# Kernel optimization log

Hardware: AMD Instinct MI355X
Metric: run time of the kernel (lower is better)

Reference implementation:

```python
import jax, jax.numpy as jnp
import numpy as np
import math

B, S, D, H = 2048, 32, 1024, 16
DK = D // H
EPS = 1e-5

def setup_inputs() -> dict:
    key = jax.random.key(0)
    ks = jax.random.split(key, 8)
    w_scale = 0.02  # realistic init scale for linear weights
    # Weights stored as (d_in, d_out): y = x @ W + b (same math as torch x @ W.T)
    return {
        "x":  jax.random.normal(ks[0], (B, S, D), jnp.float32),
        "ln_g": jnp.ones((D,), jnp.float32),
        "ln_b": jnp.zeros((D,), jnp.float32),
        "wq": jax.random.normal(ks[1], (D, D), jnp.float32) * w_scale,
        "bq": jnp.zeros((D,), jnp.float32),
        "wk": jax.random.normal(ks[2], (D, D), jnp.float32) * w_scale,
        "bk": jnp.zeros((D,), jnp.float32),
        "wv": jax.random.normal(ks[3], (D, D), jnp.float32) * w_scale,
        "bv": jnp.zeros((D,), jnp.float32),
        "wo": jax.random.normal(ks[4], (D, D), jnp.float32) * w_scale,
        "bo": jnp.zeros((D,), jnp.float32),
        "rel_bias": jax.random.normal(ks[5], (H, 32, 32), jnp.float32),
    }

def reference(x, ln_g, ln_b, wq, bq, wk, bk, wv, bv, wo, bo, rel_bias):
    b, s, d = x.shape
    h = rel_bias.shape[0]
    dk = d // h
    residual = x
    # LayerNorm (eps=1e-5)
    mu = jnp.mean(x, axis=-1, keepdims=True)
    var = jnp.mean(jnp.square(x - mu), axis=-1, keepdims=True)
    xn = (x - mu) * jax.lax.rsqrt(var + EPS) * ln_g + ln_b
    # QKV projections -> [b, h, s, dk]
    def split_heads(t):
        return t.reshape(b, s, h, dk).transpose(0, 2, 1, 3)
    Q = split_heads(xn @ wq + bq)
    K = split_heads(xn @ wk + bk)
    V = split_heads(xn @ wv + bv)
    scores = jnp.einsum('bhqd,bhkd->bhqk', Q, K) / jnp.sqrt(jnp.float32(dk))
    if s <= 32:  # static at trace time, matching the torch branch
        scores = scores + rel_bias[:, :s, :s][None]
    attn = jax.nn.softmax(scores, axis=-1)
    ctx = jnp.einsum('bhqk,bhkd->bhqd', attn, V)
    ctx = ctx.transpose(0, 2, 1, 3).reshape(b, s, d)
    out = ctx @ wo + bo  # dropout is identity in eval
    return residual + out
```

## Files before the change

kernel.cpp:

```cpp
#include <hip/hip_runtime.h>
#include <stdint.h>


typedef __attribute__((ext_vector_type(8))) short bf16x8;
typedef __attribute__((ext_vector_type(4))) float f32x4;
typedef __attribute__((ext_vector_type(16))) float f32x16;

__device__ __forceinline__ float bf2f(unsigned short u) {
    return __uint_as_float(((unsigned)u) << 16);
}
__device__ __forceinline__ unsigned short f2bf(float f) {
    unsigned u = __float_as_uint(f);
    u += 0x7FFFu + ((u >> 16) & 1u);
    return (unsigned short)(u >> 16);
}
__device__ __forceinline__ uint4 pack8(const float* f) {
    uint4 u;
    u.x = (unsigned)f2bf(f[0]) | ((unsigned)f2bf(f[1]) << 16);
    u.y = (unsigned)f2bf(f[2]) | ((unsigned)f2bf(f[3]) << 16);
    u.z = (unsigned)f2bf(f[4]) | ((unsigned)f2bf(f[5]) << 16);
    u.w = (unsigned)f2bf(f[6]) | ((unsigned)f2bf(f[7]) << 16);
    return u;
}

typedef __attribute__((address_space(3))) unsigned lds_u32;
typedef const __attribute__((address_space(1))) unsigned glb_u32;
__device__ __forceinline__ void gld16(const void* g, void* l) {
    __builtin_amdgcn_global_load_lds((glb_u32*)g, (lds_u32*)l, 16, 0, 0);
}

__global__ __launch_bounds__(256) void lnw_kernel(
    const float* __restrict__ x, const float* __restrict__ gg,
    const float* __restrict__ bb, unsigned short* __restrict__ xn,
    const float* __restrict__ wq, const float* __restrict__ wk,
    const float* __restrict__ wv, const float* __restrict__ wo,
    unsigned short* __restrict__ wcatT, unsigned short* __restrict__ woT)
{
    __shared__ unsigned short T[64 * 72];
    if (blockIdx.x >= 16384) {
        int bid = blockIdx.x - 16384;
        int p = bid >> 8;
        int t = bid & 255;
        int k0 = (t >> 4) * 64, n0 = (t & 15) * 64;
        const float* src = (p == 0) ? wq : (p == 1) ? wk : (p == 2) ? wv : wo;
        unsigned short* dst = (p < 3) ? (wcatT + (size_t)p * 1048576) : woT;
        int tid = threadIdx.x;
#pragma unroll
        for (int it = 0; it < 2; it++) {
            int flat = it * 2048 + tid * 8;
            int r = flat >> 6, c = flat & 63;
            const float* s4 = src + (size_t)(k0 + r) * 1024 + n0 + c;
            float4 u0 = *(const float4*)s4;
            float4 u1 = *(const float4*)(s4 + 4);
            float f[8] = {u0.x, u0.y, u0.z, u0.w, u1.x, u1.y, u1.z, u1.w};
            *(uint4*)&T[r * 72 + c] = pack8(f);
        }
        __syncthreads();
#pragma unroll
        for (int it = 0; it < 2; it++) {
            int flat = it * 2048 + tid * 8;
            int rn = flat >> 6, ck = flat & 63;
            unsigned short v[8];
#pragma unroll
            for (int j = 0; j < 8; j++) v[j] = T[(ck + j) * 72 + rn];
            uint4 u;
            u.x = (unsigned)v[0] | ((unsigned)v[1] << 16);
            u.y = (unsigned)v[2] | ((unsigned)v[3] << 16);
            u.z = (unsigned)v[4] | ((unsigned)v[5] << 16);
            u.w = (unsigned)v[6] | ((unsigned)v[7] << 16);
            *(uint4*)(dst + (size_t)(n0 + rn) * 1024 + k0 + ck) = u;
        }
        return;
    }
    int l = threadIdx.x & 63;
    size_t row = (size_t)blockIdx.x * 4 + (threadIdx.x >> 6);
    const float* xr = x + row * 1024;
    float f0[8], f1[8];
    *(float4*)&f0[0] = *(const float4*)(xr + l * 8);
    *(float4*)&f0[4] = *(const float4*)(xr + l * 8 + 4);
    *(float4*)&f1[0] = *(const float4*)(xr + 512 + l * 8);
    *(float4*)&f1[4] = *(const float4*)(xr + 512 + l * 8 + 4);
    float s = 0.f, s2 = 0.f;
#pragma unroll
    for (int j = 0; j < 8; j++) { s += f0[j] + f1[j]; s2 += f0[j] * f0[j] + f1[j] * f1[j]; }
#pragma unroll
    for (int m = 1; m < 64; m <<= 1) { s += __shfl_xor(s, m); s2 += __shfl_xor(s2, m); }
    float mu = s * (1.f / 1024.f);
    float var = s2 * (1.f / 1024.f) - mu * mu;
    float rs = rsqrtf(var + 1e-5f);
    float fg0[8], fg1[8], fb0[8], fb1[8];
    *(float4*)&fg0[0] = *(const float4*)(gg + l * 8);
    *(float4*)&fg0[4] = *(const float4*)(gg + l * 8 + 4);
    *(float4*)&fg1[0] = *(const float4*)(gg + 512 + l * 8);
    *(float4*)&fg1[4] = *(const float4*)(gg + 512 + l * 8 + 4);
    *(float4*)&fb0[0] = *(const float4*)(bb + l * 8);
    *(float4*)&fb0[4] = *(const float4*)(bb + l * 8 + 4);
    *(float4*)&fb1[0] = *(const float4*)(bb + 512 + l * 8);
    *(float4*)&fb1[4] = *(const float4*)(bb + 512 + l * 8 + 4);
    float o0[8], o1[8];
#pragma unroll
    for (int j = 0; j < 8; j++) {
        o0[j] = (f0[j] - mu) * rs * fg0[j] + fb0[j];
        o1[j] = (f1[j] - mu) * rs * fg1[j] + fb1[j];
    }
    *(uint4*)(xn + row * 1024 + l * 8) = pack8(o0);
    *(uint4*)(xn + row * 1024 + 512 + l * 8) = pack8(o1);
}

#define FENCE asm volatile("" ::: "memory")
#define BARRIER do { FENCE; __builtin_amdgcn_s_barrier(); FENCE; } while (0)
#define WAIT_LGKM0 do { asm volatile("s_waitcnt lgkmcnt(0)" ::: "memory"); \
                        __builtin_amdgcn_sched_barrier(0); } while (0)
#define VMCNT(n) asm volatile("s_waitcnt vmcnt(" #n ")" ::: "memory")

#define FQ_SA(buf) (LDSU + (buf) * 8192)
#define FQ_SB(buf) (LDSU + 16384 + (buf) * 12288)
#define QS_OFF 0
#define KS_OFF 9216
#define VT_OFF 18432
#define PS_OFF 28672

#define ASTG(buf, g, koff) gld16(Ag + (size_t)(g) * 32768 + (koff), \
                                 FQ_SA(buf) + ((g) * 32 + w * 8) * 64)
#define BSTG(buf, p, c, koff) gld16(((p) == 0 ? Bgq : (p) == 1 ? Bgk : Bgv) + (size_t)(c) * 32768 + (koff), \
                                    FQ_SB(buf) + ((p) * 64 + (c) * 32 + w * 8) * 64)

#define FLDA(buf, q, ks) (*(const bf16x8*)&FQ_SA(buf)[ \
    (wm * 64 + (q) * 16 + (l & 15)) * 64 + ((((ks) * 32) + khi) ^ aswz)])
#define FLDB(buf, cf, ks) (*(const bf16x8*)&FQ_SB(buf)[ \
    (wn * 96 + (cf) * 16 + (l & 15)) * 64 + ((((ks) * 32) + khi) ^ aswz)])

#define MFMA_HEX(q) do { \
    _Pragma("unroll") \
    for (int cf = 0; cf < 6; cf++) { \
        acc[q][cf] = __builtin_amdgcn_mfma_f32_16x16x32_bf16(aF0, bF[cf][0], acc[q][cf], 0, 0, 0); \
        acc[q][cf] = __builtin_amdgcn_mfma_f32_16x16x32_bf16(aF1, bF[cf][1], acc[q][cf], 0, 0, 0); \
    } } while (0)

#define FPHASE(buf, q, STAGE_STMT, TAIL_STMT) do { \
    bf16x8 aF0 = FLDA(buf, q, 0), aF1 = FLDA(buf, q, 1); \
    if ((q) == 0) { \
        _Pragma("unroll") \
        for (int cf = 0; cf < 6; cf++) { bF[cf][0] = FLDB(buf, cf, 0); bF[cf][1] = FLDB(buf, cf, 1); } \
    } \
    STAGE_STMT; \
    BARRIER; \
    WAIT_LGKM0; \
    __builtin_amdgcn_s_setprio(1); \
    MFMA_HEX(q); \
    __builtin_amdgcn_s_setprio(0); \
    TAIL_STMT; \
    BARRIER; \
} while (0)

__global__ __launch_bounds__(256, 2) void fqa2_kernel(
    const unsigned short* __restrict__ A, const unsigned short* __restrict__ wcatT,
    const float* __restrict__ bq, const float* __restrict__ bk,
    const float* __restrict__ bv, const float* __restrict__ rb,
    unsigned short* __restrict__ ctx)
{
    __shared__ __align__(16) unsigned short LDSU[40960];
    int bx = blockIdx.x;
    int h  = ((bx & 7) << 1) | ((bx >> 3) & 1);
    int mp = bx >> 4;
    int m0 = mp * 128;
    int tid = threadIdx.x, l = tid & 63, w = tid >> 6;
    int wm = w >> 1, wn = w & 1;
    int khi = (l >> 4) * 8;
    int aswz = (l & 7) * 8;
    int swzc = ((l & 7) ^ (l >> 3)) * 8;

    const unsigned short* Ag  = A + (size_t)(m0 + w * 8 + (l >> 3)) * 1024 + swzc;
    const unsigned short* Bgq = wcatT + (size_t)(h * 64 + w * 8 + (l >> 3)) * 1024 + swzc;
    const unsigned short* Bgk = Bgq + 1048576ull;
    const unsigned short* Bgv = Bgq + 2097152ull;

    f32x4 acc[4][6];
#pragma unroll
    for (int i = 0; i < 4; i++)
#pragma unroll
        for (int j = 0; j < 6; j++)
#pragma unroll
            for (int v = 0; v < 4; v++) acc[i][j][v] = 0.f;

    bf16x8 bF[6][2];

    ASTG(0, 0, 0); ASTG(0, 1, 0); ASTG(0, 2, 0); ASTG(0, 3, 0);
    BSTG(0, 0, 0, 0); BSTG(0, 0, 1, 0); BSTG(0, 1, 0, 0);
    BSTG(0, 1, 1, 0); BSTG(0, 2, 0, 0); BSTG(0, 2, 1, 0);
    BSTG(1, 0, 0, 64); BSTG(1, 0, 1, 64); BSTG(1, 1, 0, 64);
    BSTG(1, 1, 1, 64); BSTG(1, 2, 0, 64); BSTG(1, 2, 1, 64);
    VMCNT(6);
    BARRIER;

    for (int it = 0; it < 7; ++it) {
        int ko1 = (2 * it + 1) * 64, ko2 = (2 * it + 2) * 64, ko3 = (2 * it + 3) * 64;
        FPHASE(0, 0, do { ASTG(1, 0, ko1); ASTG(1, 1, ko1); } while (0), (void)0);
        FPHASE(0, 1, do { ASTG(1, 2, ko1); ASTG(1, 3, ko1); } while (0), (void)0);
        FPHASE(0, 2, do { BSTG(0, 0, 0, ko2); BSTG(0, 0, 1, ko2); BSTG(0, 1, 0, ko2); } while (0), (void)0);
        FPHASE(0, 3, do { BSTG(0, 1, 1, ko2); BSTG(0, 2, 0, ko2); BSTG(0, 2, 1, ko2); } while (0), VMCNT(6));
        FPHASE(1, 0, do { ASTG(0, 0, ko2); ASTG(0, 1, ko2); } while (0), (void)0);
        FPHASE(1, 1, do { ASTG(0, 2, ko2); ASTG(0, 3, ko2); } while (0), (void)0);
        FPHASE(1, 2, do { BSTG(1, 0, 0, ko3); BSTG(1, 0, 1, ko3); BSTG(1, 1, 0, ko3); } while (0), (void)0);
        FPHASE(1, 3, do { BSTG(1, 1, 1, ko3); BSTG(1, 2, 0, ko3); BSTG(1, 2, 1, ko3); } while (0), VMCNT(6));
    }
    FPHASE(0, 0, do { ASTG(1, 0, 960); ASTG(1, 1, 960); } while (0), (void)0);
    FPHASE(0, 1, do { ASTG(1, 2, 960); ASTG(1, 3, 960); } while (0), (void)0);
    FPHASE(0, 2, (void)0, (void)0);
    FPHASE(0, 3, (void)0, VMCNT(0));
    FPHASE(1, 0, (void)0, (void)0);
    FPHASE(1, 1, (void)0, (void)0);
    FPHASE(1, 2, (void)0, (void)0);
    FPHASE(1, 3, (void)0, (void)0);
    __builtin_amdgcn_sched_barrier(0);

#pragma unroll
    for (int cf = 0; cf < 6; cf++) {
        int colg = wn * 96 + cf * 16 + (l & 15);
        int seg = colg >> 6;
        int cseg = colg & 63;
        const float* bp = (seg == 0) ? bq : (seg == 1) ? bk : bv;
        float bias = bp[h * 64 + cseg];
#pragma unroll
        for (int ai = 0; ai < 4; ai++) {
#pragma unroll
            for (int v = 0; v < 4; v++) {
                int row = wm * 64 + ai * 16 + (l >> 4) * 4 + v;
                unsigned short val = f2bf(acc[ai][cf][v] + bias);
                if (seg == 0)      LDSU[QS_OFF + row * 72 + cseg] = val;
                else if (seg == 1) LDSU[KS_OFF + row * 72 + cseg] = val;
                else               LDSU[VT_OFF + (((row >> 5) << 6) + cseg) * 40 + (row & 31)] = val;
            }
        }
    }
    __syncthreads();

    {
        int col = l & 31, hi = l >> 5;
        f32x16 s;
#pragma unroll
        for (int i = 0; i < 16; i++) s[i] = 0.f;
#pragma unroll
        for (int t = 0; t < 4; t++) {
            bf16x8 aQ = *(const bf16x8*)&LDSU[QS_OFF + (w * 32 + col) * 72 + t * 16 + hi * 8];
            bf16x8 bK = *(const bf16x8*)&LDSU[KS_OFF + (w * 32 + col) * 72 + t * 16 + hi * 8];
            s = __builtin_amdgcn_mfma_f32_32x32x16_bf16(aQ, bK, s, 0, 0, 0);
        }
        const float* rbh = rb + h * 1024;
        unsigned short* ps = LDSU + PS_OFF + w * 1280;
#pragma unroll
        for (int r = 0; r < 16; r++) {
            int m = (r & 3) + 8 * (r >> 2) + 4 * hi;
            float v = s[r] * 0.125f + rbh[m * 32 + col];
            float mx = v;
#pragma unroll
            for (int msk = 1; msk < 32; msk <<= 1) mx = fmaxf(mx, __shfl_xor(mx, msk));
            float e = __expf(v - mx);
            float sm = e;
#pragma unroll
            for (int msk = 1; msk < 32; msk <<= 1) sm += __shfl_xor(sm, msk);
            ps[m * 40 + col] = f2bf(e / sm);
        }
        bf16x8 pa0 = *(const bf16x8*)&ps[col * 40 + hi * 8];
        bf16x8 pa1 = *(const bf16x8*)&ps[col * 40 + 16 + hi * 8];
        size_t rowb = ((size_t)mp * 4 + w) * 32;
#pragma unroll
        for (int c2 = 0; c2 < 2; c2++) {
            bf16x8 vb0 = *(const bf16x8*)&LDSU[VT_OFF + (w * 64 + c2 * 32 + col) * 40 + hi * 8];
            bf16x8 vb1 = *(const bf16x8*)&LDSU[VT_OFF + (w * 64 + c2 * 32 + col) * 40 + 16 + hi * 8];
            f32x16 o;
#pragma unroll
            for (int i = 0; i < 16; i++) o[i] = 0.f;
            o = __builtin_amdgcn_mfma_f32_32x32x16_bf16(pa0, vb0, o, 0, 0, 0);
            o = __builtin_amdgcn_mfma_f32_32x32x16_bf16(pa1, vb1, o, 0, 0, 0);
#pragma unroll
            for (int r = 0; r < 16; r++) {
                int m = (r & 3) + 8 * (r >> 2) + 4 * hi;
                ctx[(rowb + m) * 1024 + h * 64 + c2 * 32 + col] = f2bf(o[r]);
            }
        }
    }
}

#define SAp(buf) (LDSB + (buf) * 16384)
#define SBp(buf) (LDSB + 32768 + (buf) * 16384)

#define STG(gb, hh, kcol, ldsreg) do { \
    const unsigned short* _g = (gb) + (size_t)((hh) * 128) * 1024 + (kcol); \
    unsigned short* _d = (ldsreg) + ((hh) * 128 + w * 8) * 64; \
    gld16(_g, _d); gld16(_g + 64 * 1024, _d + 64 * 64); } while (0)

#define LDA(buf, q, rfq, ks) (*(const bf16x8*)&SAp(buf)[ \
    (wm * 128 + (q) * 32 + (rfq) * 16 + (l & 15)) * 64 + ((((ks) * 32) + khi) ^ aswz)])
#define LDB(buf, cf, ks) (*(const bf16x8*)&SBp(buf)[ \
    (wn * 64 + (cf) * 16 + (l & 15)) * 64 + ((((ks) * 32) + khi) ^ aswz)])

#define MFMA_QUAD(q) do { \
    _Pragma("unroll") \
    for (int cf = 0; cf < 4; cf++) { \
        acc[(q)*2+0][cf] = __builtin_amdgcn_mfma_f32_16x16x32_bf16(aF00, bF[cf][0], acc[(q)*2+0][cf], 0, 0, 0); \
        acc[(q)*2+0][cf] = __builtin_amdgcn_mfma_f32_16x16x32_bf16(aF01, bF[cf][1], acc[(q)*2+0][cf], 0, 0, 0); \
        acc[(q)*2+1][cf] = __builtin_amdgcn_mfma_f32_16x16x32_bf16(aF10, bF[cf][0], acc[(q)*2+1][cf], 0, 0, 0); \
        acc[(q)*2+1][cf] = __builtin_amdgcn_mfma_f32_16x16x32_bf16(aF11, bF[cf][1], acc[(q)*2+1][cf], 0, 0, 0); \
    } } while (0)

#define PHASE(buf, q, STAGE_STMT, TAIL_STMT) do { \
    bf16x8 aF00 = LDA(buf, q, 0, 0), aF01 = LDA(buf, q, 0, 1); \
    bf16x8 aF10 = LDA(buf, q, 1, 0), aF11 = LDA(buf, q, 1, 1); \
    if ((q) == 0) { \
        _Pragma("unroll") \
        for (int cf = 0; cf < 4; cf++) { bF[cf][0] = LDB(buf, cf, 0); bF[cf][1] = LDB(buf, cf, 1); } \
    } \
    STAGE_STMT; \
    BARRIER; \
    WAIT_LGKM0; \
    __builtin_amdgcn_s_setprio(1); \
    MFMA_QUAD(q); \
    __builtin_amdgcn_s_setprio(0); \
    TAIL_STMT; \
    BARRIER; \
} while (0)

__global__ __launch_bounds__(512, 2) void gemm8res(
    const unsigned short* __restrict__ A, const unsigned short* __restrict__ Bt,
    const float* __restrict__ bz0, const float* __restrict__ resid,
    float* __restrict__ out, int NTL)
{
    __shared__ __align__(16) unsigned short LDSB[65536];
    int cpx = gridDim.x >> 3;
    int bid = (blockIdx.x & 7) * cpx + (blockIdx.x >> 3);
    int mt = bid / NTL, ntl = bid % NTL;
    int m0 = mt * 256, n0 = ntl * 256;
    int tid = threadIdx.x, l = tid & 63, w = tid >> 6;
    int wm = w >> 2, wn = w & 3;
    int khi = (l >> 4) * 8;
    int aswz = (l & 7) * 8;

    const unsigned short* Ag = A + (size_t)(m0 + w * 8 + (l >> 3)) * 1024 + ((l & 7) ^ (l >> 3)) * 8;
    const unsigned short* Bg = Bt + (size_t)(n0 + w * 8 + (l >> 3)) * 1024 + ((l & 7) ^ (l >> 3)) * 8;
    unsigned short* sA0 = SAp(0);
    unsigned short* sA1 = SAp(1);
    unsigned short* sB0 = SBp(0);
    unsigned short* sB1 = SBp(1);

    f32x4 acc[8][4];
#pragma unroll
    for (int i = 0; i < 8; i++)
#pragma unroll
        for (int j = 0; j < 4; j++)
#pragma unroll
            for (int v = 0; v < 4; v++) acc[i][j][v] = 0.f;

    bf16x8 bF[4][2];

    STG(Ag, 0, 0, sA0); STG(Ag, 1, 0, sA0);
    STG(Bg, 0, 0, sB0); STG(Bg, 1, 0, sB0);
    STG(Bg, 0, 64, sB1); STG(Bg, 1, 64, sB1);
    VMCNT(4);
    BARRIER;

    for (int it = 0; it < 7; ++it) {
        int koff = it * 128;
        PHASE(0, 0, STG(Ag, 0, koff + 64, sA1), (void)0);
        PHASE(0, 1, STG(Ag, 1, koff + 64, sA1), (void)0);
        PHASE(0, 2, STG(Bg, 0, koff + 128, sB0), (void)0);
        PHASE(0, 3, STG(Bg, 1, koff + 128, sB0), VMCNT(4));
        PHASE(1, 0, STG(Ag, 0, koff + 128, sA0), (void)0);
        PHASE(1, 1, STG(Ag, 1, koff + 128, sA0), (void)0);
        PHASE(1, 2, STG(Bg, 0, koff + 192, sB1), (void)0);
        PHASE(1, 3, STG(Bg, 1, koff + 192, sB1), VMCNT(4));
    }
    PHASE(0, 0, STG(Ag, 0, 960, sA1), (void)0);
    PHASE(0, 1, STG(Ag, 1, 960, sA1), (void)0);
    PHASE(0, 2, (void)0, (void)0);
    PHASE(0, 3, (void)0, VMCNT(0));
    PHASE(1, 0, (void)0, (void)0);
    PHASE(1, 1, (void)0, (void)0);
    PHASE(1, 2, (void)0, (void)0);
    PHASE(1, 3, (void)0, (void)0);
    __builtin_amdgcn_sched_barrier(0);

    float* Cf = (float*)LDSB;
    int gcol = n0 + l * 4;
    float4 bzv = *(const float4*)(bz0 + gcol);
#pragma unroll
    for (int pass = 0; pass < 2; pass++) {
        __syncthreads();
#pragma unroll
        for (int rfq = 0; rfq < 4; rfq++) {
            int rf = pass * 4 + rfq;
#pragma unroll
            for (int cf = 0; cf < 4; cf++) {
                int c0 = wn * 64 + cf * 16 + (l & 15);
                int c4 = c0 >> 2, ce = c0 & 3;
#pragma unroll
                for (int v = 0; v < 4; v++) {
                    int rl = wm * 64 + rfq * 16 + (l >> 4) * 4 + v;
                    Cf[rl * 256 + ((c4 ^ (rl & 7)) << 2) + ce] = acc[rf][cf][v];
                }
            }
        }
        __syncthreads();
#pragma unroll
        for (int rb4 = 0; rb4 < 4; rb4++) {
            float4 rz[4], cv[4];
#pragma unroll
            for (int k = 0; k < 4; k++) {
                int rr = (rb4 * 4 + k) * 8 + w;
                int grow = m0 + (rr & 63) + ((rr >> 6) << 7) + pass * 64;
                rz[k] = *(const float4*)(resid + (size_t)grow * 1024 + gcol);
            }
#pragma unroll
            for (int k = 0; k < 4; k++) {
                int rr = (rb4 * 4 + k) * 8 + w;
                cv[k] = *(const float4*)&Cf[rr * 256 + ((l ^ (rr & 7)) << 2)];
            }
#pragma unroll
            for (int k = 0; k < 4; k++) {
                int rr = (rb4 * 4 + k) * 8 + w;
                int grow = m0 + (rr & 63) + ((rr >> 6) << 7) + pass * 64;
                float4 o;
                o.x = cv[k].x + bzv.x + rz[k].x;
                o.y = cv[k].y + bzv.y + rz[k].y;
                o.z = cv[k].z + bzv.z + rz[k].z;
                o.w = cv[k].w + bzv.w + rz[k].w;
                *(float4*)(out + (size_t)grow * 1024 + gcol) = o;
            }
        }
    }
}

extern "C" void kernel_launch(void* const* d_in, const int* in_sizes, int n_in,
                              void* d_out, int out_size, void* d_ws, size_t ws_size,
                              hipStream_t stream)
{
    const float* x  = (const float*)d_in[0];
    const float* lg = (const float*)d_in[1];
    const float* lb = (const float*)d_in[2];
    const float* wq = (const float*)d_in[3];
    const float* bq = (const float*)d_in[4];
    const float* wk = (const float*)d_in[5];
    const float* bk = (const float*)d_in[6];
    const float* wv = (const float*)d_in[7];
    const float* bv = (const float*)d_in[8];
    const float* wo = (const float*)d_in[9];
    const float* bo = (const float*)d_in[10];
    const float* rb = (const float*)d_in[11];
    float* out = (float*)d_out;
    unsigned short* ws = (unsigned short*)d_ws;

    unsigned short* wcatT = ws;
    unsigned short* woT   = wcatT + 3145728;
    unsigned short* xn    = woT + 1048576;
    unsigned short* ctx   = xn + 67108864ull;

    lnw_kernel<<<dim3(17408), dim3(256), 0, stream>>>(
        x, lg, lb, xn, wq, wk, wv, wo, wcatT, woT);

    fqa2_kernel<<<dim3(8192), dim3(256), 0, stream>>>(xn, wcatT, bq, bk, bv, rb, ctx);

    gemm8res<<<dim3(1024), dim3(512), 0, stream>>>(ctx, woT, bo, x, out, 4);
}
```

Measured before the change: 761.8 us.

## Merge GEMM phases into paired quads and stage ctx output through LDS

The fused QKV+attention kernel now handles two A row-quads per phase. This halves the number of barrier-separated phases in the K loop and issues larger groups of global-to-LDS staging loads per phase. The attention epilogue computes both 32-column PV halves together, writes them to the warp's V^T LDS region, and then stores ctx with 16-byte coalesced writes instead of scattered 2-byte stores. Two A fragments stay live at once, which raises register pressure, and reusing the V^T region for output assumes each warp only touches its own slice.

Result: faster. 744.5 us (-2.3%).

```diff
diff --git a/kernel.cpp b/kernel.cpp
--- a/kernel.cpp
+++ b/kernel.cpp
@@ -130,16 +130,17 @@
 #define FLDB(buf, cf, ks) (*(const bf16x8*)&FQ_SB(buf)[ \
     (wn * 96 + (cf) * 16 + (l & 15)) * 64 + ((((ks) * 32) + khi) ^ aswz)])
 
-#define MFMA_HEX(q) do { \
+#define MFMA_HEX2(q, a0, a1) do { \
     _Pragma("unroll") \
     for (int cf = 0; cf < 6; cf++) { \
-        acc[q][cf] = __builtin_amdgcn_mfma_f32_16x16x32_bf16(aF0, bF[cf][0], acc[q][cf], 0, 0, 0); \
-        acc[q][cf] = __builtin_amdgcn_mfma_f32_16x16x32_bf16(aF1, bF[cf][1], acc[q][cf], 0, 0, 0); \
+        acc[q][cf] = __builtin_amdgcn_mfma_f32_16x16x32_bf16(a0, bF[cf][0], acc[q][cf], 0, 0, 0); \
+        acc[q][cf] = __builtin_amdgcn_mfma_f32_16x16x32_bf16(a1, bF[cf][1], acc[q][cf], 0, 0, 0); \
     } } while (0)
 
-#define FPHASE(buf, q, STAGE_STMT, TAIL_STMT) do { \
-    bf16x8 aF0 = FLDA(buf, q, 0), aF1 = FLDA(buf, q, 1); \
-    if ((q) == 0) { \
+#define FPHASE2(buf, q0, LOADB, STAGE_STMT, TAIL_STMT) do { \
+    bf16x8 aF0 = FLDA(buf, q0, 0), aF1 = FLDA(buf, q0, 1); \
+    bf16x8 aG0 = FLDA(buf, (q0) + 1, 0), aG1 = FLDA(buf, (q0) + 1, 1); \
+    if (LOADB) { \
         _Pragma("unroll") \
         for (int cf = 0; cf < 6; cf++) { bF[cf][0] = FLDB(buf, cf, 0); bF[cf][1] = FLDB(buf, cf, 1); } \
     } \
@@ -147,7 +148,8 @@
     BARRIER; \
     WAIT_LGKM0; \
     __builtin_amdgcn_s_setprio(1); \
-    MFMA_HEX(q); \
+    MFMA_HEX2(q0, aF0, aF1); \
+    MFMA_HEX2((q0) + 1, aG0, aG1); \
     __builtin_amdgcn_s_setprio(0); \
     TAIL_STMT; \
     BARRIER; \
@@ -195,23 +197,27 @@
 
     for (int it = 0; it < 7; ++it) {
         int ko1 = (2 * it + 1) * 64, ko2 = (2 * it + 2) * 64, ko3 = (2 * it + 3) * 64;
-        FPHASE(0, 0, do { ASTG(1, 0, ko1); ASTG(1, 1, ko1); } while (0), (void)0);
-        FPHASE(0, 1, do { ASTG(1, 2, ko1); ASTG(1, 3, ko1); } while (0), (void)0);
-        FPHASE(0, 2, do { BSTG(0, 0, 0, ko2); BSTG(0, 0, 1, ko2); BSTG(0, 1, 0, ko2); } while (0), (void)0);
-        FPHASE(0, 3, do { BSTG(0, 1, 1, ko2); BSTG(0, 2, 0, ko2); BSTG(0, 2, 1, ko2); } while (0), VMCNT(6));
-        FPHASE(1, 0, do { ASTG(0, 0, ko2); ASTG(0, 1, ko2); } while (0), (void)0);
-        FPHASE(1, 1, do { ASTG(0, 2, ko2); ASTG(0, 3, ko2); } while (0), (void)0);
-        FPHASE(1, 2, do { BSTG(1, 0, 0, ko3); BSTG(1, 0, 1, ko3); BSTG(1, 1, 0, ko3); } while (0), (void)0);
-        FPHASE(1, 3, do { BSTG(1, 1, 1, ko3); BSTG(1, 2, 0, ko3); BSTG(1, 2, 1, ko3); } while (0), VMCNT(6));
-    }
-    FPHASE(0, 0, do { ASTG(1, 0, 960); ASTG(1, 1, 960); } while (0), (void)0);
-    FPHASE(0, 1, do { ASTG(1, 2, 960); ASTG(1, 3, 960); } while (0), (void)0);
-    FPHASE(0, 2, (void)0, (void)0);
-    FPHASE(0, 3, (void)0, VMCNT(0));
-    FPHASE(1, 0, (void)0, (void)0);
-    FPHASE(1, 1, (void)0, (void)0);
-    FPHASE(1, 2, (void)0, (void)0);
-    FPHASE(1, 3, (void)0, (void)0);
+        FPHASE2(0, 0, 1,
+            do { ASTG(1, 0, ko1); ASTG(1, 1, ko1); ASTG(1, 2, ko1); ASTG(1, 3, ko1); } while (0),
+            (void)0);
+        FPHASE2(0, 2, 0,
+            do { BSTG(0, 0, 0, ko2); BSTG(0, 0, 1, ko2); BSTG(0, 1, 0, ko2);
+                 BSTG(0, 1, 1, ko2); BSTG(0, 2, 0, ko2); BSTG(0, 2, 1, ko2); } while (0),
+            VMCNT(6));
+        FPHASE2(1, 0, 1,
+            do { ASTG(0, 0, ko2); ASTG(0, 1, ko2); ASTG(0, 2, ko2); ASTG(0, 3, ko2); } while (0),
+            (void)0);
+        FPHASE2(1, 2, 0,
+            do { BSTG(1, 0, 0, ko3); BSTG(1, 0, 1, ko3); BSTG(1, 1, 0, ko3);
+                 BSTG(1, 1, 1, ko3); BSTG(1, 2, 0, ko3); BSTG(1, 2, 1, ko3); } while (0),
+            VMCNT(6));
+    }
+    FPHASE2(0, 0, 1,
+        do { ASTG(1, 0, 960); ASTG(1, 1, 960); ASTG(1, 2, 960); ASTG(1, 3, 960); } while (0),
+        (void)0);
+    FPHASE2(0, 2, 0, (void)0, VMCNT(0));
+    FPHASE2(1, 0, 1, (void)0, (void)0);
+    FPHASE2(1, 2, 0, (void)0, (void)0);
     __builtin_amdgcn_sched_barrier(0);
 
 #pragma unroll
@@ -261,23 +267,34 @@
             for (int msk = 1; msk < 32; msk <<= 1) sm += __shfl_xor(sm, msk);
             ps[m * 40 + col] = f2bf(e / sm);
         }
+        unsigned short* vtw = LDSU + VT_OFF + w * 2560;
         bf16x8 pa0 = *(const bf16x8*)&ps[col * 40 + hi * 8];
         bf16x8 pa1 = *(const bf16x8*)&ps[col * 40 + 16 + hi * 8];
+        bf16x8 vb00 = *(const bf16x8*)&vtw[(col) * 40 + hi * 8];
+        bf16x8 vb01 = *(const bf16x8*)&vtw[(col) * 40 + 16 + hi * 8];
+        bf16x8 vb10 = *(const bf16x8*)&vtw[(32 + col) * 40 + hi * 8];
+        bf16x8 vb11 = *(const bf16x8*)&vtw[(32 + col) * 40 + 16 + hi * 8];
+        f32x16 o0, o1;
+#pragma unroll
+        for (int i = 0; i < 16; i++) { o0[i] = 0.f; o1[i] = 0.f; }
+        o0 = __builtin_amdgcn_mfma_f32_32x32x16_bf16(pa0, vb00, o0, 0, 0, 0);
+        o0 = __builtin_amdgcn_mfma_f32_32x32x16_bf16(pa1, vb01, o0, 0, 0, 0);
+        o1 = __builtin_amdgcn_mfma_f32_32x32x16_bf16(pa0, vb10, o1, 0, 0, 0);
+        o1 = __builtin_amdgcn_mfma_f32_32x32x16_bf16(pa1, vb11, o1, 0, 0, 0);
+
+#pragma unroll
+        for (int r = 0; r < 16; r++) {
+            int m = (r & 3) + 8 * (r >> 2) + 4 * hi;
+            vtw[m * 72 + col]      = f2bf(o0[r]);
+            vtw[m * 72 + 32 + col] = f2bf(o1[r]);
+        }
         size_t rowb = ((size_t)mp * 4 + w) * 32;
 #pragma unroll
-        for (int c2 = 0; c2 < 2; c2++) {
-            bf16x8 vb0 = *(const bf16x8*)&LDSU[VT_OFF + (w * 64 + c2 * 32 + col) * 40 + hi * 8];
-            bf16x8 vb1 = *(const bf16x8*)&LDSU[VT_OFF + (w * 64 + c2 * 32 + col) * 40 + 16 + hi * 8];
-            f32x16 o;
-#pragma unroll
-            for (int i = 0; i < 16; i++) o[i] = 0.f;
-            o = __builtin_amdgcn_mfma_f32_32x32x16_bf16(pa0, vb0, o, 0, 0, 0);
-            o = __builtin_amdgcn_mfma_f32_32x32x16_bf16(pa1, vb1, o, 0, 0, 0);
-#pragma unroll
-            for (int r = 0; r < 16; r++) {
-                int m = (r & 3) + 8 * (r >> 2) + 4 * hi;
-                ctx[(rowb + m) * 1024 + h * 64 + c2 * 32 + col] = f2bf(o[r]);
-            }
+        for (int pass = 0; pass < 4; pass++) {
+            int row = pass * 8 + (l >> 3);
+            int c = (l & 7) * 8;
+            uint4 val = *(const uint4*)&vtw[row * 72 + c];
+            *(uint4*)(ctx + (rowb + row) * 1024 + h * 64 + c) = val;
         }
     }
 }
```
